# Kernel tuning notes

Measured on AMD Instinct MI355X. Metric: run time of the kernel, lower is better.

## Reference

```python
import jax, jax.numpy as jnp
import numpy as np

N, L, C, K = 8, 16384, 256, 64  # batch, points, d_color, anchor_num; d_struct = 4*K = 256


def setup_inputs() -> dict:
    key = jax.random.key(0)
    ks = jax.random.split(key, 12)
    d_in = C + 4 * K  # 512
    s1, s2, s3 = 1.0 / np.sqrt(d_in), 1.0 / np.sqrt(128), 1.0 / np.sqrt(256)
    return {
        'feat0': jax.random.normal(ks[0], (N, L, C), jnp.float32),
        'feat1': jax.random.normal(ks[1], (N, L, C), jnp.float32),
        'pts_3d0': jax.random.normal(ks[2], (N, L, 3), jnp.float32),
        'pts_3d1': jax.random.normal(ks[3], (N, L, 3), jnp.float32),
        'anchor_i': jax.random.randint(ks[4], (N, K), 0, L, jnp.int32),
        'anchor_j': jax.random.randint(ks[5], (N, K), 0, L, jnp.int32),
        'W1': jax.random.uniform(ks[6], (d_in, 128), jnp.float32, -s1, s1),
        'b1': jax.random.uniform(ks[7], (128,), jnp.float32, -s1, s1),
        'W2': jax.random.uniform(ks[8], (128, 256), jnp.float32, -s2, s2),
        'b2': jax.random.uniform(ks[9], (256,), jnp.float32, -s2, s2),
        'W3': jax.random.uniform(ks[10], (256, C), jnp.float32, -s3, s3),
        'b3': jax.random.uniform(ks[11], (C,), jnp.float32, -s3, s3),
    }


def _structured(pts, anchor_idx):
    # pts: [N,L,3], anchor_idx: [N,K] -> [N,L,4K]
    anchors = jnp.take_along_axis(pts, anchor_idx[:, :, None], axis=1)  # [N,K,3]
    diff = pts[:, :, None, :] - anchors[:, None, :, :]                  # [N,L,K,3]
    dist = jnp.sum(diff * diff, axis=-1, keepdims=True)                 # [N,L,K,1]
    f = jnp.concatenate([diff, dist], axis=-1)                          # [N,L,K,4]
    f = f / jnp.sum(jnp.abs(f), axis=-2, keepdims=True)                 # L1 norm over K
    f = jnp.swapaxes(f, -1, -2).reshape(pts.shape[0], pts.shape[1], -1)  # [N,L,4K]
    # original l1_norm is @torch.no_grad -> structured feature is detached
    return jax.lax.stop_gradient(f)


def _mlp(x, W1, b1, W2, b2, W3, b3):
    h = jax.nn.relu(x @ W1 + b1)
    h = jax.nn.relu(h @ W2 + b2)  # dropout is identity in eval
    return h @ W3 + b3


def reference(feat0, feat1, pts_3d0, pts_3d1, anchor_i, anchor_j,
              W1, b1, W2, b2, W3, b3):
    s0 = _structured(pts_3d0, anchor_i)
    s1 = _structured(pts_3d1, anchor_j)
    aug0 = _mlp(jnp.concatenate([feat0, s0], axis=-1), W1, b1, W2, b2, W3, b3)
    aug1 = _mlp(jnp.concatenate([feat1, s1], axis=-1), W1, b1, W2, b2, W3, b3)
    return aug0, aug1
```

## Files before the change

kernel.cpp:

```cpp
#include <hip/hip_runtime.h>

typedef __bf16 bf16x8 __attribute__((ext_vector_type(8)));
typedef float f32x4 __attribute__((ext_vector_type(4)));
typedef unsigned short u16x4 __attribute__((ext_vector_type(4)));

#define NBATCH 8
#define LPTS   16384
#define CDIM   256
#define KANC   64
#define DIN    512
#define H1DIM  128
#define H2DIM  256
#define TM     64

__device__ __forceinline__ unsigned short f2b(float f){
  __bf16 h = (__bf16)f;
  return __builtin_bit_cast(unsigned short, h);
}

__global__ __launch_bounds__(256) void prep_weights(
    const float* __restrict__ W1, const float* __restrict__ W2,
    const float* __restrict__ W3, unsigned short* __restrict__ wt){
  int id = blockIdx.x * 256 + threadIdx.x;
  if (id < 65536){
    int r = id >> 9, c = id & 511;
    wt[id] = f2b(W1[c * 128 + r]);
  } else if (id < 98304){
    int t = id - 65536; int r = t >> 7, c = t & 127;
    wt[id] = f2b(W2[c * 256 + r]);
  } else if (id < 163840){
    int t = id - 98304; int r = t >> 8, c = t & 255;
    wt[id] = f2b(W3[c * 256 + r]);
  }
}

__global__ __launch_bounds__(128) void prep_coef(
    const float* __restrict__ pts0, const float* __restrict__ pts1,
    const int* __restrict__ anc_i, const int* __restrict__ anc_j,
    const float* __restrict__ W1, float* __restrict__ coef){
  const int comb = blockIdx.x;
  const int strm = comb >> 3, n = comb & 7;
  const int col  = threadIdx.x;
  __shared__ float4 anc[64];
  const float* pts  = strm ? pts1 : pts0;
  const int*   anci = strm ? anc_j : anc_i;
  if (col < 64){
    int ai = anci[n * KANC + col];
    const float* ap = pts + ((size_t)n * LPTS + ai) * 3;
    anc[col] = make_float4(ap[0], ap[1], ap[2], 0.f);
  }
  __syncthreads();
  float SX=0,CX=0,SY=0,CY=0,SZ=0,CZ=0,SD=0,ADx=0,ADy=0,ADz=0,CD2=0;
  float SAx=0,SAy=0,SAz=0,SA2=0;
  for (int k = 0; k < KANC; ++k){
    float4 a = anc[k];
    float ak2 = a.x*a.x + a.y*a.y + a.z*a.z;
    float wx = W1[(256 + k) * 128 + col];
    float wy = W1[(320 + k) * 128 + col];
    float wz = W1[(384 + k) * 128 + col];
    float wd = W1[(448 + k) * 128 + col];
    SX += wx; CX += a.x * wx;
    SY += wy; CY += a.y * wy;
    SZ += wz; CZ += a.z * wz;
    SD += wd; ADx += a.x * wd; ADy += a.y * wd; ADz += a.z * wd;
    CD2 += ak2 * wd;
    SAx += a.x; SAy += a.y; SAz += a.z; SA2 += ak2;
  }
  float* cf = coef + (size_t)comb * 12 * 128;
  cf[ 0*128+col]=SX;  cf[ 1*128+col]=CX;  cf[ 2*128+col]=SY;  cf[ 3*128+col]=CY;
  cf[ 4*128+col]=SZ;  cf[ 5*128+col]=CZ;  cf[ 6*128+col]=SD;  cf[ 7*128+col]=ADx;
  cf[ 8*128+col]=ADy; cf[ 9*128+col]=ADz; cf[10*128+col]=CD2;
  if (col == 0) cf[11*128+0] = SAx;
  if (col == 1) cf[11*128+1] = SAy;
  if (col == 2) cf[11*128+2] = SAz;
  if (col == 3) cf[11*128+3] = SA2;
}

__global__ __launch_bounds__(512, 6) void fused(
    const float* __restrict__ feat0, const float* __restrict__ feat1,
    const float* __restrict__ pts0, const float* __restrict__ pts1,
    const int* __restrict__ anc_i, const int* __restrict__ anc_j,
    const float* __restrict__ b1, const float* __restrict__ b2,
    const float* __restrict__ b3, const unsigned short* __restrict__ wt,
    const float* __restrict__ coef, float* __restrict__ out)
{
  __shared__ unsigned short xs[TM * 256];
  __shared__ unsigned short h1s[TM * H1DIM];
  __shared__ float scal[TM][12];
  unsigned short* h2s = xs;
  float4* anc4 = (float4*)h1s;

  const int tid  = threadIdx.x;
  const int wg   = blockIdx.x;
  const int strm = wg >> 11;
  const int n    = (wg >> 8) & 7;
  const int l0   = (wg & 255) * TM;

  const float* feat = strm ? feat1 : feat0;
  const float* pts  = strm ? pts1 : pts0;
  const int*   anci = strm ? anc_j : anc_i;
  const float* cf   = coef + (size_t)((strm << 3) | n) * 12 * 128;

  const float* pp = pts + ((size_t)n * LPTS + l0 + (tid >> 3)) * 3;
  float px = pp[0], py = pp[1], pz = pp[2];
  float SAx = cf[11*128+0], SAy = cf[11*128+1], SAz = cf[11*128+2], SA2 = cf[11*128+3];

  if (tid < KANC){
    int ai = anci[n * KANC + tid];
    const float* ap = pts + ((size_t)n * LPTS + ai) * 3;
    anc4[tid + (tid >> 3)] = make_float4(ap[0], ap[1], ap[2], 0.f);
  }

  {
    const float4* fb = (const float4*)(feat + ((size_t)n * LPTS + l0) * CDIM);
    #pragma unroll
    for (int it = 0; it < 8; ++it){
      int flat = it * 512 + tid;
      int r = flat >> 6, c4 = flat & 63;
      float4 v = fb[flat];
      int e = (r * 256 + c4 * 4) ^ ((r & 7) << 3);
      u16x4 pk = { f2b(v.x), f2b(v.y), f2b(v.z), f2b(v.w) };
      *(u16x4*)&xs[e] = pk;
    }
  }
  __syncthreads();

  {
    const int l   = tid >> 3;
    const int sub = tid & 7;
    float s0 = 0.f, s1 = 0.f, s2 = 0.f;
    #pragma unroll
    for (int i = 0; i < 8; ++i){
      float4 a = anc4[sub * 9 + i];
      s0 += fabsf(px - a.x); s1 += fabsf(py - a.y); s2 += fabsf(pz - a.z);
    }
    #pragma unroll
    for (int m = 1; m <= 4; m <<= 1){
      s0 += __shfl_xor(s0, m, 64);
      s1 += __shfl_xor(s1, m, 64);
      s2 += __shfl_xor(s2, m, 64);
    }
    float pp2 = px*px + py*py + pz*pz;
    float s3 = 64.f * pp2 - 2.f * (px*SAx + py*SAy + pz*SAz) + SA2;
    float i0 = 1.f/s0, i1 = 1.f/s1, i2 = 1.f/s2, i3 = 1.f/s3;
    float u;
    switch (sub){
      case 0: u = i0 * px;       break;
      case 1: u = -i0;           break;
      case 2: u = i1 * py;       break;
      case 3: u = -i1;           break;
      case 4: u = i2 * pz;       break;
      case 5: u = -i2;           break;
      case 6: u = i3 * pp2;      break;
      default: u = -2.f*i3*px;   break;
    }
    scal[l][sub] = u;
    if (sub < 3){
      float u2 = (sub == 0) ? -2.f*i3*py : (sub == 1) ? -2.f*i3*pz : i3;
      scal[l][8 + sub] = u2;
    }
  }
  __syncthreads();

  const int lane = tid & 63;
  const int w    = tid >> 6;
  const int lr   = lane & 15;
  const int lg   = lane >> 4;

  {
    f32x4 acc[4] = {};
    const int col = w * 16 + lr;
    const unsigned short* wrow = wt + col * DIN;
    float cc[11];
    #pragma unroll
    for (int j = 0; j < 11; ++j) cc[j] = cf[j * 128 + col];
    #pragma unroll 4
    for (int kk = 0; kk < 8; ++kk){
      int kb = kk * 32 + lg * 8;
      bf16x8 b = *(const bf16x8*)&wrow[kb];
      #pragma unroll
      for (int m = 0; m < 4; ++m){
        int row = m * 16 + lr;
        bf16x8 a = *(const bf16x8*)&xs[(row * 256 + kb) ^ ((row & 7) << 3)];
        acc[m] = __builtin_amdgcn_mfma_f32_16x16x32_bf16(a, b, acc[m], 0, 0, 0);
      }
    }
    float bias = b1[col];
    #pragma unroll
    for (int m = 0; m < 4; ++m){
      #pragma unroll
      for (int r = 0; r < 4; ++r){
        int row = m * 16 + lg * 4 + r;
        f32x4 ua = *(const f32x4*)&scal[row][0];
        f32x4 ub = *(const f32x4*)&scal[row][4];
        f32x4 uc = *(const f32x4*)&scal[row][8];
        float s = acc[m][r] + bias;
        s += ua[0]*cc[0] + ua[1]*cc[1] + ua[2]*cc[2] + ua[3]*cc[3];
        s += ub[0]*cc[4] + ub[1]*cc[5] + ub[2]*cc[6] + ub[3]*cc[7];
        s += uc[0]*cc[8] + uc[1]*cc[9] + uc[2]*cc[10];
        float v = fmaxf(s, 0.f);
        h1s[(row * H1DIM + col) ^ ((row & 7) << 3)] = f2b(v);
      }
    }
  }
  __syncthreads();

  {
    const unsigned short* w2t = wt + 65536;
    f32x4 acc[4][2] = {};
    const int col0 = w * 32;
    #pragma unroll
    for (int kk = 0; kk < 4; ++kk){
      int kb = kk * 32 + lg * 8;
      bf16x8 bf0 = *(const bf16x8*)&w2t[(col0 + lr) * H1DIM + kb];
      bf16x8 bf1 = *(const bf16x8*)&w2t[(col0 + 16 + lr) * H1DIM + kb];
      #pragma unroll
      for (int m = 0; m < 4; ++m){
        int row = m * 16 + lr;
        bf16x8 a = *(const bf16x8*)&h1s[(row * H1DIM + kb) ^ ((row & 7) << 3)];
        acc[m][0] = __builtin_amdgcn_mfma_f32_16x16x32_bf16(a, bf0, acc[m][0], 0, 0, 0);
        acc[m][1] = __builtin_amdgcn_mfma_f32_16x16x32_bf16(a, bf1, acc[m][1], 0, 0, 0);
      }
    }
    #pragma unroll
    for (int nt = 0; nt < 2; ++nt){
      int col = col0 + nt * 16 + lr;
      float bias = b2[col];
      #pragma unroll
      for (int m = 0; m < 4; ++m){
        #pragma unroll
        for (int r = 0; r < 4; ++r){
          int row = m * 16 + lg * 4 + r;
          float v = fmaxf(acc[m][nt][r] + bias, 0.f);
          h2s[(row * H2DIM + col) ^ ((row & 7) << 3)] = f2b(v);
        }
      }
    }
  }
  __syncthreads();

  {
    const unsigned short* w3t = wt + 98304;
    f32x4 acc[4][2] = {};
    const int col0 = w * 32;
    #pragma unroll 4
    for (int kk = 0; kk < 8; ++kk){
      int kb = kk * 32 + lg * 8;
      bf16x8 bf0 = *(const bf16x8*)&w3t[(col0 + lr) * H2DIM + kb];
      bf16x8 bf1 = *(const bf16x8*)&w3t[(col0 + 16 + lr) * H2DIM + kb];
      #pragma unroll
      for (int m = 0; m < 4; ++m){
        int row = m * 16 + lr;
        bf16x8 a = *(const bf16x8*)&h2s[(row * H2DIM + kb) ^ ((row & 7) << 3)];
        acc[m][0] = __builtin_amdgcn_mfma_f32_16x16x32_bf16(a, bf0, acc[m][0], 0, 0, 0);
        acc[m][1] = __builtin_amdgcn_mfma_f32_16x16x32_bf16(a, bf1, acc[m][1], 0, 0, 0);
      }
    }
    float* ob = out + (((size_t)strm * NBATCH + n) * LPTS + l0) * CDIM;
    #pragma unroll
    for (int nt = 0; nt < 2; ++nt){
      int col = col0 + nt * 16 + lr;
      float bias = b3[col];
      #pragma unroll
      for (int m = 0; m < 4; ++m){
        #pragma unroll
        for (int r = 0; r < 4; ++r){
          int row = m * 16 + lg * 4 + r;
          ob[(size_t)row * CDIM + col] = acc[m][nt][r] + bias;
        }
      }
    }
  }
}

extern "C" void kernel_launch(void* const* d_in, const int* in_sizes, int n_in,
                              void* d_out, int out_size, void* d_ws, size_t ws_size,
                              hipStream_t stream){
  const float* feat0 = (const float*)d_in[0];
  const float* feat1 = (const float*)d_in[1];
  const float* pts0  = (const float*)d_in[2];
  const float* pts1  = (const float*)d_in[3];
  const int*   anci  = (const int*)d_in[4];
  const int*   ancj  = (const int*)d_in[5];
  const float* W1    = (const float*)d_in[6];
  const float* b1    = (const float*)d_in[7];
  const float* W2    = (const float*)d_in[8];
  const float* b2    = (const float*)d_in[9];
  const float* W3    = (const float*)d_in[10];
  const float* b3    = (const float*)d_in[11];
  unsigned short* wt = (unsigned short*)d_ws;
  float* coef = (float*)((char*)d_ws + 163840 * sizeof(unsigned short));
  float* out = (float*)d_out;

  prep_weights<<<640, 256, 0, stream>>>(W1, W2, W3, wt);
  prep_coef<<<16, 128, 0, stream>>>(pts0, pts1, anci, ancj, W1, coef);
  fused<<<4096, 512, 0, stream>>>(feat0, feat1, pts0, pts1, anci, ancj,
                                  b1, b2, b3, wt, coef, out);
}
```

Before: 234.6 us.

## Prefetch first weight fragments early and use LDS-only barriers

Replaces __syncthreads with a custom barrier that waits only on LDS/scalar counters (lgkmcnt), so outstanding global loads need not drain at each barrier. The first k-slice of the W1, W2 and W3 fragments is loaded at kernel entry so their latency overlaps the feature staging and structured-feature math. To fit the extra live registers, the occupancy hint drops from 6 to 4 waves per SIMD. The risk is lower occupancy and, if the compiler does not insert vmcnt waits itself, ordering assumptions around global loads.

```diff
diff --git a/kernel.cpp b/kernel.cpp
--- a/kernel.cpp
+++ b/kernel.cpp
@@ -17,6 +17,12 @@
   __bf16 h = (__bf16)f;
   return __builtin_bit_cast(unsigned short, h);
 }
+
+#define LBAR() do{ \
+  asm volatile("s_waitcnt lgkmcnt(0)" ::: "memory"); \
+  __builtin_amdgcn_s_barrier(); \
+  asm volatile("" ::: "memory"); \
+} while(0)
 
 __global__ __launch_bounds__(256) void prep_weights(
     const float* __restrict__ W1, const float* __restrict__ W2,
@@ -76,7 +82,7 @@
   if (col == 3) cf[11*128+3] = SA2;
 }
 
-__global__ __launch_bounds__(512, 6) void fused(
+__global__ __launch_bounds__(512, 4) void fused(
     const float* __restrict__ feat0, const float* __restrict__ feat1,
     const float* __restrict__ pts0, const float* __restrict__ pts1,
     const int* __restrict__ anc_i, const int* __restrict__ anc_j,
@@ -101,6 +107,22 @@
   const int*   anci = strm ? anc_j : anc_i;
   const float* cf   = coef + (size_t)((strm << 3) | n) * 12 * 128;
 
+  const int lane = tid & 63;
+  const int w    = tid >> 6;
+  const int lr   = lane & 15;
+  const int lg   = lane >> 4;
+  const int col1 = w * 16 + lr;
+  const int col0 = w * 32;
+  const unsigned short* wrow1 = wt + col1 * DIN;
+  const unsigned short* w2t = wt + 65536;
+  const unsigned short* w3t = wt + 98304;
+
+  bf16x8 g1b = *(const bf16x8*)&wrow1[lg * 8];
+  bf16x8 g2b0 = *(const bf16x8*)&w2t[(col0      + lr) * H1DIM + lg * 8];
+  bf16x8 g2b1 = *(const bf16x8*)&w2t[(col0 + 16 + lr) * H1DIM + lg * 8];
+  bf16x8 g3b0 = *(const bf16x8*)&w3t[(col0      + lr) * H2DIM + lg * 8];
+  bf16x8 g3b1 = *(const bf16x8*)&w3t[(col0 + 16 + lr) * H2DIM + lg * 8];
+
   const float* pp = pts + ((size_t)n * LPTS + l0 + (tid >> 3)) * 3;
   float px = pp[0], py = pp[1], pz = pp[2];
   float SAx = cf[11*128+0], SAy = cf[11*128+1], SAz = cf[11*128+2], SA2 = cf[11*128+3];
@@ -123,7 +145,7 @@
       *(u16x4*)&xs[e] = pk;
     }
   }
-  __syncthreads();
+  LBAR();
 
   {
     const int l   = tid >> 3;
@@ -160,24 +182,17 @@
       scal[l][8 + sub] = u2;
     }
   }
-  __syncthreads();
-
-  const int lane = tid & 63;
-  const int w    = tid >> 6;
-  const int lr   = lane & 15;
-  const int lg   = lane >> 4;
+  LBAR();
 
   {
     f32x4 acc[4] = {};
-    const int col = w * 16 + lr;
-    const unsigned short* wrow = wt + col * DIN;
     float cc[11];
     #pragma unroll
-    for (int j = 0; j < 11; ++j) cc[j] = cf[j * 128 + col];
+    for (int j = 0; j < 11; ++j) cc[j] = cf[j * 128 + col1];
     #pragma unroll 4
     for (int kk = 0; kk < 8; ++kk){
       int kb = kk * 32 + lg * 8;
-      bf16x8 b = *(const bf16x8*)&wrow[kb];
+      bf16x8 b = (kk == 0) ? g1b : *(const bf16x8*)&wrow1[kb];
       #pragma unroll
       for (int m = 0; m < 4; ++m){
         int row = m * 16 + lr;
@@ -185,7 +200,7 @@
         acc[m] = __builtin_amdgcn_mfma_f32_16x16x32_bf16(a, b, acc[m], 0, 0, 0);
       }
     }
-    float bias = b1[col];
+    float bias = b1[col1];
     #pragma unroll
     for (int m = 0; m < 4; ++m){
       #pragma unroll
@@ -199,21 +214,19 @@
         s += ub[0]*cc[4] + ub[1]*cc[5] + ub[2]*cc[6] + ub[3]*cc[7];
         s += uc[0]*cc[8] + uc[1]*cc[9] + uc[2]*cc[10];
         float v = fmaxf(s, 0.f);
-        h1s[(row * H1DIM + col) ^ ((row & 7) << 3)] = f2b(v);
-      }
-    }
-  }
-  __syncthreads();
-
-  {
-    const unsigned short* w2t = wt + 65536;
+        h1s[(row * H1DIM + col1) ^ ((row & 7) << 3)] = f2b(v);
+      }
+    }
+  }
+  LBAR();
+
+  {
     f32x4 acc[4][2] = {};
-    const int col0 = w * 32;
     #pragma unroll
     for (int kk = 0; kk < 4; ++kk){
       int kb = kk * 32 + lg * 8;
-      bf16x8 bf0 = *(const bf16x8*)&w2t[(col0 + lr) * H1DIM + kb];
-      bf16x8 bf1 = *(const bf16x8*)&w2t[(col0 + 16 + lr) * H1DIM + kb];
+      bf16x8 bf0 = (kk == 0) ? g2b0 : *(const bf16x8*)&w2t[(col0 + lr) * H1DIM + kb];
+      bf16x8 bf1 = (kk == 0) ? g2b1 : *(const bf16x8*)&w2t[(col0 + 16 + lr) * H1DIM + kb];
       #pragma unroll
       for (int m = 0; m < 4; ++m){
         int row = m * 16 + lr;
@@ -237,17 +250,15 @@
       }
     }
   }
-  __syncthreads();
-
-  {
-    const unsigned short* w3t = wt + 98304;
+  LBAR();
+
+  {
     f32x4 acc[4][2] = {};
-    const int col0 = w * 32;
     #pragma unroll 4
     for (int kk = 0; kk < 8; ++kk){
       int kb = kk * 32 + lg * 8;
-      bf16x8 bf0 = *(const bf16x8*)&w3t[(col0 + lr) * H2DIM + kb];
-      bf16x8 bf1 = *(const bf16x8*)&w3t[(col0 + 16 + lr) * H2DIM + kb];
+      bf16x8 bf0 = (kk == 0) ? g3b0 : *(const bf16x8*)&w3t[(col0 + lr) * H2DIM + kb];
+      bf16x8 bf1 = (kk == 0) ? g3b1 : *(const bf16x8*)&w3t[(col0 + 16 + lr) * H2DIM + kb];
       #pragma unroll
       for (int m = 0; m < 4; ++m){
         int row = m * 16 + lr;
```

After: 210.6 us. 1.11x faster.
